# Kernel optimization log

Hardware: AMD Instinct MI355X
Metric: run time of the kernel (lower is better)

## Reference

```python
import jax, jax.numpy as jnp
import numpy as np

DT = 0.01
KKT_REG = 1e-3  # small Tikhonov regularization for the all-active KKT proxy


def _forward(x, v, cld, dist, mu, cor, Minv):
    bs, n, d = x.shape  # d == 2
    nc = cld.shape[1]
    nd = n * d
    i, j = cld[..., 0], cld[..., 1]
    # contact point positions (n_p == 1 so object == point)
    p1 = jnp.take_along_axis(x, i[..., None], axis=1)  # [bs, nc, 2]
    p2 = jnp.take_along_axis(x, j[..., None], axis=1)
    diff = p2 - p1
    e_n = diff / jnp.linalg.norm(diff, axis=-1, keepdims=True)  # contact normal
    e_t = jnp.stack([-e_n[..., 1], e_n[..., 0]], axis=-1)       # tangent (d=2)
    # contact Jacobian [bs, nc, 2(normal/tangent), n, d]; c_tilde == 1 for n_p=1
    bi = jnp.arange(bs)[:, None]
    ci = jnp.arange(nc)[None, :]
    Jac = jnp.zeros((bs, nc, 2, n, d), x.dtype)
    Jac = Jac.at[bi, ci, 0, i].set(-e_n)
    Jac = Jac.at[bi, ci, 0, j].set(e_n)
    Jac = Jac.at[bi, ci, 1, i].set(-e_t)
    Jac = Jac.at[bi, ci, 1, j].set(e_t)
    J_cn = Jac[:, :, 0].reshape(bs, nc, nd)          # normal rows
    Jt = Jac[:, :, 1].reshape(bs, nc, nd)            # tangent rows
    # interleaved +/- tangent rows: J_ct[0::2]=Jt, J_ct[1::2]=-Jt
    J_ct = jnp.stack([Jt, -Jt], axis=2).reshape(bs, 2 * nc, nd)
    M = jnp.linalg.inv(Minv)
    pM = jnp.kron(M, jnp.eye(d, dtype=x.dtype))      # populated_M[i::d, i::d] = M
    E = jnp.kron(jnp.eye(nc, dtype=x.dtype), jnp.ones((2, 1), x.dtype))  # [2nc, nc]
    vflat = v.reshape(bs, nd)
    Mv = vflat @ pM.T
    Jcnv = jnp.einsum('bcj,bj->bc', J_cn, vflat)
    v_star0 = -dist / DT / 8.0
    h = jnp.concatenate([jnp.minimum(-v_star0, cor * Jcnv),
                         jnp.zeros((bs, 3 * nc), x.dtype)], axis=1)  # [bs, 4nc]
    G = jnp.concatenate([J_cn, J_ct, jnp.zeros((bs, nc, nd), x.dtype)], axis=1)
    m = 4 * nc
    F = jnp.zeros((bs, m, m), x.dtype)
    F = F.at[:, 3 * nc:, :nc].set(jax.vmap(jnp.diag)(mu))
    F = F.at[:, nc:3 * nc, 3 * nc:].set(E)
    F = F.at[:, 3 * nc:, nc:3 * nc].set(-E.T)
    # lcp_solver(pM, Mv, G, h, [], [], -F) replaced by the all-active KKT solve:
    #   [pM  G^T] [z]   [-Mv]
    #   [G   -F ] [l] = [-h ]
    K = jnp.zeros((bs, nd + m, nd + m), x.dtype)
    K = K.at[:, :nd, :nd].set(pM)
    K = K.at[:, :nd, nd:].set(jnp.swapaxes(G, 1, 2))
    K = K.at[:, nd:, :nd].set(G)
    K = K.at[:, nd:, nd:].set(-F)
    K = K + KKT_REG * jnp.eye(nd + m, dtype=x.dtype)
    rhs = jnp.concatenate([-Mv, -h], axis=1)
    sol = jnp.linalg.solve(K, rhs[..., None])[..., 0]
    v_plus = -sol[:, :nd]
    # torch.stack([x, new_v], 1).reshape(bs, -1)
    return jnp.concatenate([x.reshape(bs, nd), v_plus], axis=1)


def setup_inputs() -> dict:
    key = jax.random.key(0)
    ks = jax.random.split(key, 8)
    bs, n, nc = 1024, 64, 32
    x = jax.random.normal(ks[0], (bs, n, 2), jnp.float32)
    v = jax.random.normal(ks[1], (bs, n, 2), jnp.float32)
    i = jax.random.randint(ks[2], (bs, nc), 0, n // 2)
    j = jax.random.randint(ks[3], (bs, nc), n // 2, n)
    cld_ij_ids = jnp.stack([i, j], axis=-1).astype(jnp.int32)
    dist_ij = -0.1 * jax.random.uniform(ks[4], (bs, nc), jnp.float32)
    mu = jax.random.uniform(ks[5], (bs, nc), jnp.float32)
    cor = jax.random.uniform(ks[6], (bs, nc), jnp.float32)
    A = jax.random.normal(ks[7], (n, n), jnp.float32)
    Minv = A @ A.T / n + jnp.eye(n, dtype=jnp.float32)  # SPD inverse mass matrix
    return {"x": x, "v": v, "cld_ij_ids": cld_ij_ids, "dist_ij": dist_ij,
            "mu": mu, "cor": cor, "Minv": Minv}


def reference(x, v, cld_ij_ids, dist_ij, mu, cor, Minv):
    return _forward(x, v, cld_ij_ids, dist_ij, mu, cor, Minv)
```

## Files before the change

### kernel.cpp

```cpp
#include <hip/hip_runtime.h>
#include <math.h>


#define NBODY 64
#define NC    32
#define ND    128
#define EPS   1e-3f
#define WPAD  65

__device__ __forceinline__ float readlane_f(float x, int lane) {
  return __int_as_float(__builtin_amdgcn_readlane(__float_as_int(x), lane));
}

__device__ __forceinline__ float rcp_fast(float x) {
  float r;
  asm("v_rcp_f32 %0, %1" : "=v"(r) : "v"(x));
  return r;
}

__global__ __launch_bounds__(64) void precompute_W(
    const float* __restrict__ Minv, float* __restrict__ Wg) {
  const int lane = threadIdx.x;
  const int col = blockIdx.x;

  float Mr[NBODY];
  const float4* mv = (const float4*)(Minv + lane * NBODY);
#pragma unroll
  for (int e4 = 0; e4 < 16; ++e4) {
    float4 t = mv[e4];
    Mr[4 * e4] = t.x; Mr[4 * e4 + 1] = t.y;
    Mr[4 * e4 + 2] = t.z; Mr[4 * e4 + 3] = t.w;
  }

  const float dlt = (lane == col) ? 1.0f : 0.0f;
  float s = dlt;
#pragma unroll
  for (int t = 0; t < 6; ++t) {
    float a0 = 0.f, a1 = 0.f, a2 = 0.f, a3 = 0.f;
#pragma unroll
    for (int e = 0; e < NBODY; e += 4) {
      a0 = fmaf(Mr[e],     readlane_f(s, e),     a0);
      a1 = fmaf(Mr[e + 1], readlane_f(s, e + 1), a1);
      a2 = fmaf(Mr[e + 2], readlane_f(s, e + 2), a2);
      a3 = fmaf(Mr[e + 3], readlane_f(s, e + 3), a3);
    }
    s = dlt - EPS * ((a0 + a1) + (a2 + a3));
  }
  float a0 = 0.f, a1 = 0.f, a2 = 0.f, a3 = 0.f;
#pragma unroll
  for (int e = 0; e < NBODY; e += 4) {
    a0 = fmaf(Mr[e],     readlane_f(s, e),     a0);
    a1 = fmaf(Mr[e + 1], readlane_f(s, e + 1), a1);
    a2 = fmaf(Mr[e + 2], readlane_f(s, e + 2), a2);
    a3 = fmaf(Mr[e + 3], readlane_f(s, e + 3), a3);
  }
  Wg[lane * NBODY + col] = (a0 + a1) + (a2 + a3);
}

__global__ __launch_bounds__(256, 2) void solve_batch(
    const float* __restrict__ x, const float* __restrict__ v,
    const int* __restrict__ cld, const float* __restrict__ dist,
    const float* __restrict__ cor, const float* __restrict__ Wg,
    float* __restrict__ out) {
  __shared__ float Wl[NBODY * WPAD];
  __shared__ float vw_[2][ND];
  __shared__ float qw_[2][ND];
  __shared__ float yw_[2][ND];
  __shared__ float mb_[2][2][64];
  __shared__ float dv_[2][64];

  const int tid  = threadIdx.x;
  const int wave = tid >> 6;
  const int lane = tid & 63;
  const int pair = wave >> 1;
  const int wp   = wave & 1;
  const int b    = blockIdx.x * 2 + pair;

  for (int idx = tid; idx < NBODY * NBODY; idx += 256)
    Wl[(idx >> 6) * WPAD + (idx & 63)] = Wg[idx];

  const float* xb = x + b * ND;
  const float* vb = v + b * ND;
  float* vw = vw_[pair];
  float* qw = qw_[pair];
  float* yw = yw_[pair];
  float* mb0 = mb_[pair][0];
  float* mb1 = mb_[pair][1];
  float* dv = dv_[pair];

  const int t = lane + 64 * wp;
  vw[t] = vb[t];

  const int rc = lane & 31;
  const int myi = cld[b * 2 * NC + 2 * rc];
  const int myj = cld[b * 2 * NC + 2 * rc + 1];
  float dx = xb[2 * myj]     - xb[2 * myi];
  float dy = xb[2 * myj + 1] - xb[2 * myi + 1];
  float il = 1.0f / sqrtf(dx * dx + dy * dy);
  float enx = dx * il, eny = dy * il;
  float wx = (lane < 32) ? enx : -eny;
  float wy = (lane < 32) ? eny : enx;
  __syncthreads();

  const int kc = lane & 1;
  const int a  = t >> 1;
  const float* Wa = Wl + a * WPAD;
  {
    float s = 0.f;
    for (int e = 0; e < NBODY; ++e) s = fmaf(Wa[e], vw[2 * e + kc], s);
    qw[t] = vw[t] - EPS * s;
  }
  __syncthreads();

  float rhs;
  {
    float qdx = qw[2 * myj]     - qw[2 * myi];
    float qdy = qw[2 * myj + 1] - qw[2 * myi + 1];
    float h = 0.0f;
    if (lane < 32) {
      float vdx = vw[2 * myj]     - vw[2 * myi];
      float vdy = vw[2 * myj + 1] - vw[2 * myi + 1];
      float jcnv = enx * vdx + eny * vdy;
      h = fminf(dist[b * NC + rc] * 12.5f, cor[b * NC + rc] * jcnv);
    }
    rhs = h - (wx * qdx + wy * qdy);
  }

  float rowh[32];
  const float* Wi = Wl + myi * WPAD;
  const float* Wj = Wl + myj * WPAD;
#pragma unroll
  for (int tt = 0; tt < 32; ++tt) {
    int c = 2 * tt + wp;
    int ic = __builtin_amdgcn_readlane(myi, c);
    int jc = __builtin_amdgcn_readlane(myj, c);
    float wcx = readlane_f(wx, c);
    float wcy = readlane_f(wy, c);
    float kap = (Wi[ic] - Wi[jc]) - (Wj[ic] - Wj[jc]);
    float aa = (wx * wcx + wy * wcy) * kap;
    aa = (c == lane) ? aa - ((lane < 32) ? EPS : 0.5f * EPS) : aa;
    rowh[tt] = aa;
  }

#pragma unroll
  for (int k = 0; k < 64; ++k) {
    const int ow = k & 1;
    float m;
    if (wp == ow) {
      float pv = readlane_f(rowh[k >> 1], k);
      float r0 = rcp_fast(pv);
      m = (lane == k) ? 0.0f : rowh[k >> 1] * r0;
      (ow ? mb1 : mb0)[lane] = m;
      if (lane == k) dv[k] = r0;
    }
    __syncthreads();
    if (wp != ow) m = (ow ? mb1 : mb0)[lane];
    rhs = fmaf(-m, readlane_f(rhs, k), rhs);
#pragma unroll
    for (int tt = (k >> 1); tt < 32; ++tt)
      rowh[tt] = fmaf(-m, readlane_f(rowh[tt], k), rowh[tt]);
  }

  float myx = rhs * dv[lane];

  {
    float y = 0.f;
#pragma unroll
    for (int c = 0; c < 32; ++c) {
      float ex = readlane_f(wx, c),      ey = readlane_f(wy, c);
      float tx = readlane_f(wx, c + 32), ty = readlane_f(wy, c + 32);
      float lam = readlane_f(myx, c);
      float del = readlane_f(myx, c + 32);
      float wk = (kc ? ey : ex) * lam + (kc ? ty : tx) * del;
      if (wp == 0) {
        int ic = __builtin_amdgcn_readlane(myi, c);
        y -= (ic == a) ? wk : 0.0f;
      } else {
        int jc = __builtin_amdgcn_readlane(myj, c);
        y += (jc == a) ? wk : 0.0f;
      }
    }
    yw[t] = y;
  }
  __syncthreads();

  {
    float s = 0.f;
    for (int e = 0; e < NBODY; ++e) s = fmaf(Wa[e], yw[2 * e + kc], s);
    float* ob = out + b * 256;
    ob[t]       = xb[t];
    ob[128 + t] = qw[t] + s;
  }
}

extern "C" void kernel_launch(void* const* d_in, const int* in_sizes, int n_in,
                              void* d_out, int out_size, void* d_ws, size_t ws_size,
                              hipStream_t stream) {
  const float* x    = (const float*)d_in[0];
  const float* v    = (const float*)d_in[1];
  const int*   cld  = (const int*)  d_in[2];
  const float* dist = (const float*)d_in[3];
  const float* cor  = (const float*)d_in[5];
  const float* Minv = (const float*)d_in[6];
  float* out = (float*)d_out;

  const int bs = in_sizes[0] / ND;
  float* W = (float*)d_ws;

  precompute_W<<<NBODY, 64, 0, stream>>>(Minv, W);
  solve_batch<<<bs / 2, 256, 0, stream>>>(x, v, cld, dist, cor, W, out);
}
```

Before: 95.02 us.

## Split each batch solve across four waves with blocked 4-pivot elimination

Each 256-thread block now handles one batch element instead of two. The 64 KKT-proxy columns are distributed across four waves instead of two. Gaussian elimination is blocked into groups of four pivots, so the owning wave factors four pivots locally and publishes a float4 of multipliers. This needs one block barrier per four pivots instead of one per pivot, and each wave holds fewer register columns. The cost is twice as many blocks, each redoing the 16KB W load into LDS, and idle waves 2-3 during the final phases.

```diff
diff --git a/kernel.cpp b/kernel.cpp
--- a/kernel.cpp
+++ b/kernel.cpp
@@ -57,39 +57,30 @@
   Wg[lane * NBODY + col] = (a0 + a1) + (a2 + a3);
 }
 
-__global__ __launch_bounds__(256, 2) void solve_batch(
+__global__ __launch_bounds__(256, 4) void solve_batch(
     const float* __restrict__ x, const float* __restrict__ v,
     const int* __restrict__ cld, const float* __restrict__ dist,
     const float* __restrict__ cor, const float* __restrict__ Wg,
     float* __restrict__ out) {
   __shared__ float Wl[NBODY * WPAD];
-  __shared__ float vw_[2][ND];
-  __shared__ float qw_[2][ND];
-  __shared__ float yw_[2][ND];
-  __shared__ float mb_[2][2][64];
-  __shared__ float dv_[2][64];
+  __shared__ float vw[ND], qw[ND], yw[ND];
+  __shared__ float4 mrow[2][64];
+  __shared__ float dv[64];
 
   const int tid  = threadIdx.x;
-  const int wave = tid >> 6;
+  const int w    = tid >> 6;
   const int lane = tid & 63;
-  const int pair = wave >> 1;
-  const int wp   = wave & 1;
-  const int b    = blockIdx.x * 2 + pair;
+  const int b    = blockIdx.x;
 
   for (int idx = tid; idx < NBODY * NBODY; idx += 256)
     Wl[(idx >> 6) * WPAD + (idx & 63)] = Wg[idx];
 
   const float* xb = x + b * ND;
   const float* vb = v + b * ND;
-  float* vw = vw_[pair];
-  float* qw = qw_[pair];
-  float* yw = yw_[pair];
-  float* mb0 = mb_[pair][0];
-  float* mb1 = mb_[pair][1];
-  float* dv = dv_[pair];
-
-  const int t = lane + 64 * wp;
-  vw[t] = vb[t];
+
+  const int half = w & 1;
+  const int t = lane + 64 * half;
+  if (w < 2) vw[t] = vb[t];
 
   const int rc = lane & 31;
   const int myi = cld[b * 2 * NC + 2 * rc];
@@ -100,16 +91,34 @@
   float enx = dx * il, eny = dy * il;
   float wx = (lane < 32) ? enx : -eny;
   float wy = (lane < 32) ? eny : enx;
+
   __syncthreads();
 
   const int kc = lane & 1;
   const int a  = t >> 1;
   const float* Wa = Wl + a * WPAD;
-  {
+  if (w < 2) {
     float s = 0.f;
     for (int e = 0; e < NBODY; ++e) s = fmaf(Wa[e], vw[2 * e + kc], s);
     qw[t] = vw[t] - EPS * s;
   }
+
+  float rowq[16];
+  const float* Wi = Wl + myi * WPAD;
+  const float* Wj = Wl + myj * WPAD;
+#pragma unroll
+  for (int q = 0; q < 16; ++q) {
+    int c = 16 * (q >> 2) + 4 * w + (q & 3);
+    int ic = __builtin_amdgcn_readlane(myi, c);
+    int jc = __builtin_amdgcn_readlane(myj, c);
+    float wcx = readlane_f(wx, c);
+    float wcy = readlane_f(wy, c);
+    float kap = (Wi[ic] - Wi[jc]) - (Wj[ic] - Wj[jc]);
+    float aa = (wx * wcx + wy * wcy) * kap;
+    aa = (c == lane) ? aa - ((lane < 32) ? EPS : 0.5f * EPS) : aa;
+    rowq[q] = aa;
+  }
+
   __syncthreads();
 
   float rhs;
@@ -126,53 +135,84 @@
     rhs = h - (wx * qdx + wy * qdy);
   }
 
-  float rowh[32];
-  const float* Wi = Wl + myi * WPAD;
-  const float* Wj = Wl + myj * WPAD;
-#pragma unroll
-  for (int tt = 0; tt < 32; ++tt) {
-    int c = 2 * tt + wp;
-    int ic = __builtin_amdgcn_readlane(myi, c);
-    int jc = __builtin_amdgcn_readlane(myj, c);
-    float wcx = readlane_f(wx, c);
-    float wcy = readlane_f(wy, c);
-    float kap = (Wi[ic] - Wi[jc]) - (Wj[ic] - Wj[jc]);
-    float aa = (wx * wcx + wy * wcy) * kap;
-    aa = (c == lane) ? aa - ((lane < 32) ? EPS : 0.5f * EPS) : aa;
-    rowh[tt] = aa;
-  }
-
-#pragma unroll
-  for (int k = 0; k < 64; ++k) {
-    const int ow = k & 1;
-    float m;
-    if (wp == ow) {
-      float pv = readlane_f(rowh[k >> 1], k);
-      float r0 = rcp_fast(pv);
-      m = (lane == k) ? 0.0f : rowh[k >> 1] * r0;
-      (ow ? mb1 : mb0)[lane] = m;
-      if (lane == k) dv[k] = r0;
+#pragma unroll
+  for (int g = 0; g < 16; ++g) {
+    const int om = g & 3;
+    const int gc = g >> 2;
+    float m0, m1, m2, m3;
+    if (w == om) {
+      const int base = 4 * gc;
+      {
+        const int k = 4 * g;
+        float r = rcp_fast(readlane_f(rowq[base], k));
+        if (lane == k) dv[k] = r;
+        m0 = (lane == k) ? 0.f : rowq[base] * r;
+        rowq[base+1] = fmaf(-m0, readlane_f(rowq[base+1], k), rowq[base+1]);
+        rowq[base+2] = fmaf(-m0, readlane_f(rowq[base+2], k), rowq[base+2]);
+        rowq[base+3] = fmaf(-m0, readlane_f(rowq[base+3], k), rowq[base+3]);
+      }
+      {
+        const int k = 4 * g + 1;
+        float r = rcp_fast(readlane_f(rowq[base+1], k));
+        if (lane == k) dv[k] = r;
+        m1 = (lane == k) ? 0.f : rowq[base+1] * r;
+        rowq[base+2] = fmaf(-m1, readlane_f(rowq[base+2], k), rowq[base+2]);
+        rowq[base+3] = fmaf(-m1, readlane_f(rowq[base+3], k), rowq[base+3]);
+      }
+      {
+        const int k = 4 * g + 2;
+        float r = rcp_fast(readlane_f(rowq[base+2], k));
+        if (lane == k) dv[k] = r;
+        m2 = (lane == k) ? 0.f : rowq[base+2] * r;
+        rowq[base+3] = fmaf(-m2, readlane_f(rowq[base+3], k), rowq[base+3]);
+      }
+      {
+        const int k = 4 * g + 3;
+        float r = rcp_fast(readlane_f(rowq[base+3], k));
+        if (lane == k) dv[k] = r;
+        m3 = (lane == k) ? 0.f : rowq[base+3] * r;
+      }
+      mrow[g & 1][lane] = make_float4(m0, m1, m2, m3);
     }
     __syncthreads();
-    if (wp != ow) m = (ow ? mb1 : mb0)[lane];
-    rhs = fmaf(-m, readlane_f(rhs, k), rhs);
-#pragma unroll
-    for (int tt = (k >> 1); tt < 32; ++tt)
-      rowh[tt] = fmaf(-m, readlane_f(rowh[tt], k), rowh[tt]);
-  }
+    if (w != om) {
+      float4 mv = mrow[g & 1][lane];
+      m0 = mv.x; m1 = mv.y; m2 = mv.z; m3 = mv.w;
+    }
+    rhs = fmaf(-m0, readlane_f(rhs, 4 * g),     rhs);
+    rhs = fmaf(-m1, readlane_f(rhs, 4 * g + 1), rhs);
+    rhs = fmaf(-m2, readlane_f(rhs, 4 * g + 2), rhs);
+    rhs = fmaf(-m3, readlane_f(rhs, 4 * g + 3), rhs);
+#pragma unroll
+    for (int cl = 0; cl < 4; ++cl) {
+      if (cl < gc) continue;
+      if ((cl > gc) || (w > om)) {
+#pragma unroll
+        for (int within = 0; within < 4; ++within) {
+          const int q = 4 * cl + within;
+          rowq[q] = fmaf(-m0, readlane_f(rowq[q], 4 * g),     rowq[q]);
+          rowq[q] = fmaf(-m1, readlane_f(rowq[q], 4 * g + 1), rowq[q]);
+          rowq[q] = fmaf(-m2, readlane_f(rowq[q], 4 * g + 2), rowq[q]);
+          rowq[q] = fmaf(-m3, readlane_f(rowq[q], 4 * g + 3), rowq[q]);
+        }
+      }
+    }
+  }
+
+  if (w >= 2) return;
 
   float myx = rhs * dv[lane];
 
   {
     float y = 0.f;
 #pragma unroll
-    for (int c = 0; c < 32; ++c) {
+    for (int c = 0; c < NC; ++c) {
       float ex = readlane_f(wx, c),      ey = readlane_f(wy, c);
       float tx = readlane_f(wx, c + 32), ty = readlane_f(wy, c + 32);
       float lam = readlane_f(myx, c);
       float del = readlane_f(myx, c + 32);
       float wk = (kc ? ey : ex) * lam + (kc ? ty : tx) * del;
-      if (wp == 0) {
+      if (w == 0) {
         int ic = __builtin_amdgcn_readlane(myi, c);
         y -= (ic == a) ? wk : 0.0f;
       } else {
@@ -208,5 +248,5 @@
   float* W = (float*)d_ws;
 
   precompute_W<<<NBODY, 64, 0, stream>>>(Minv, W);
-  solve_batch<<<bs / 2, 256, 0, stream>>>(x, v, cld, dist, cor, W, out);
-}
+  solve_batch<<<bs, 256, 0, stream>>>(x, v, cld, dist, cor, W, out);
+}
```

Measured after the change: 93.37 us. About the same (-1.7%).
